# Optimization experiments

Hardware: AMD Instinct MI355X
Metric: run time of the kernel (lower is better)

## Reference

```python
import jax, jax.numpy as jnp
import numpy as np

S = 8192          # past KV length
H = 4096          # hidden size
NH = 32           # heads
HD = 128          # head dim
INNER = 16384     # MLP inner (4h)
ROT = 64          # rotary dim per 2D-rope half
NUM_LAYERS = 28
LAYER_ID = 0
ALPHA = (2.0 * NUM_LAYERS) ** 0.5
QK_COEFF = float(LAYER_ID + 1)            # query_key_layer_scaling_coeff
COEFF = (128.0 ** 0.5) * QK_COEFF         # math.sqrt(128) * coeff
EPS = 1e-5


def layernorm(x, w, b):
    mu = jnp.mean(x, axis=-1, keepdims=True)
    var = jnp.var(x, axis=-1, keepdims=True)
    return (x - mu) * jax.lax.rsqrt(var + EPS) * w + b


def rotate_half(x):
    # x: [..., 64]; GLM rotate-half at 32
    return jnp.concatenate([-x[..., 32:], x[..., :32]], axis=-1)


def setup_inputs() -> dict:
    key = jax.random.key(0)
    ks = jax.random.split(key, 16)
    # rotary cache (as in the driver script)
    inv_freq = 1.0 / (10000.0 ** (jnp.arange(0, ROT, 2, dtype=jnp.float32) / ROT))  # [32]
    t = jnp.arange(512, dtype=jnp.float32)
    freqs = jnp.einsum('i,j->ij', t, inv_freq)          # [512,32]
    emb = jnp.concatenate([freqs, freqs], axis=-1)      # [512,64]
    w = lambda k, shp: jax.random.normal(k, shp, dtype=jnp.float32) * 0.02
    return {
        'hidden_states': jax.random.normal(ks[0], (1, H), dtype=jnp.float32),
        'past_key': jax.random.normal(ks[1], (S, NH, HD), dtype=jnp.float32),
        'past_value': jax.random.normal(ks[2], (S, NH, HD), dtype=jnp.float32),
        'cos_cached': jnp.cos(emb),
        'sin_cached': jnp.sin(emb),
        'ln1_w': jnp.ones((H,), jnp.float32), 'ln1_b': jnp.zeros((H,), jnp.float32),
        'qkv_w': w(ks[3], (3 * H, H)), 'qkv_b': w(ks[4], (3 * H,)),
        'dense_w': w(ks[5], (H, H)), 'dense_b': w(ks[6], (H,)),
        'ln2_w': jnp.ones((H,), jnp.float32), 'ln2_b': jnp.zeros((H,), jnp.float32),
        'fc1_w': w(ks[7], (INNER, H)), 'fc1_b': w(ks[8], (INNER,)),
        'fc2_w': w(ks[9], (H, INNER)), 'fc2_b': w(ks[10], (H,)),
        'position_ids': jax.random.randint(ks[11], (1, 1), 0, 512),
        'block_position_ids': jax.random.randint(ks[12], (1, 1), 0, 512),
        'attention_mask': jnp.zeros((1, 1, S + 1), dtype=bool),
    }


def reference(hidden_states, past_key, past_value, cos_cached, sin_cached,
              ln1_w, ln1_b, qkv_w, qkv_b, dense_w, dense_b,
              ln2_w, ln2_b, fc1_w, fc1_b, fc2_w, fc2_b,
              position_ids, block_position_ids, attention_mask):
    # rotary lookups: embedding then transpose(0,1) -> [q_len,1,64]
    pos_cos = jnp.transpose(cos_cached[position_ids], (1, 0, 2))
    pos_sin = jnp.transpose(sin_cached[position_ids], (1, 0, 2))
    blk_cos = jnp.transpose(cos_cached[block_position_ids], (1, 0, 2))
    blk_sin = jnp.transpose(sin_cached[block_position_ids], (1, 0, 2))

    residual = layernorm(hidden_states, ln1_w, ln1_b)          # [1, H]
    qkv = residual @ qkv_w.T + qkv_b                           # [1, 3H]
    qkv = qkv.reshape(-1, NH, 3 * HD)                          # [1, 32, 384]
    query, key_new, value_new = jnp.split(qkv, 3, axis=2)      # each [1,32,128]

    q1, q2 = jnp.split(query, 2, axis=2)                       # [1,32,64] each
    k1, k2 = jnp.split(key_new, 2, axis=2)
    q1 = q1 * pos_cos + rotate_half(q1) * pos_sin
    k1 = k1 * pos_cos + rotate_half(k1) * pos_sin
    q2 = q2 * blk_cos + rotate_half(q2) * blk_sin
    k2 = k2 * blk_cos + rotate_half(k2) * blk_sin
    q = jnp.concatenate([q1, q2], axis=-1)                     # [1,32,128]
    k_new = jnp.concatenate([k1, k2], axis=-1)                 # [1,32,128]

    k = jnp.concatenate([past_key, k_new], axis=0)             # [S+1,32,128]
    v = jnp.concatenate([past_value, value_new], axis=0)       # [S+1,32,128]

    # scores: [heads, q=1, S+1]
    scores = jnp.einsum('qhd,khd->hqk', q / COEFF, k)
    scores = jnp.where(attention_mask, jnp.float32(-10000.0), scores)
    scores = scores * QK_COEFF
    probs = jax.nn.softmax(scores, axis=-1)
    ctx = jnp.einsum('hqk,khd->qhd', probs, v).reshape(-1, H)  # [1,4096]

    attn_out = ctx @ dense_w.T + dense_b
    hidden = residual * ALPHA + attn_out

    residual2 = layernorm(hidden, ln2_w, ln2_b)
    mlp = jax.nn.gelu(residual2 @ fc1_w.T + fc1_b, approximate=True)
    mlp = mlp @ fc2_w.T + fc2_b
    out = residual2 * ALPHA + mlp
    return (out, k, v)
```

## Files before the change

### kernel.cpp

```cpp
#include <hip/hip_runtime.h>
#include <math.h>

#define S_PAST 8192
#define S_TOT  8193
#define HID    4096
#define NH     32
#define HD     128
#define INNER  16384
#define CH     16
#define NCH    512
#define ALPHA_ 7.483314773547883f
#define INV_COEFF 0.08838834764831845f
#define EPS_ 1e-5f

typedef float vf4 __attribute__((ext_vector_type(4)));

__global__ __launch_bounds__(256) void ln_kernel(const float* __restrict__ xin,
                                                 const float* __restrict__ w,
                                                 const float* __restrict__ b,
                                                 float* __restrict__ out) {
    int tid = threadIdx.x;
    float xs[16];
    float s = 0.f, s2 = 0.f;
#pragma unroll
    for (int i = 0; i < 16; ++i) {
        float v = xin[tid + i * 256];
        xs[i] = v; s += v; s2 += v * v;
    }
    for (int off = 32; off; off >>= 1) {
        s  += __shfl_down(s, off, 64);
        s2 += __shfl_down(s2, off, 64);
    }
    __shared__ float rs[4], rs2[4];
    __shared__ float mu_s, ri_s;
    int wid = tid >> 6, lane = tid & 63;
    if (lane == 0) { rs[wid] = s; rs2[wid] = s2; }
    __syncthreads();
    if (tid == 0) {
        float S1 = rs[0] + rs[1] + rs[2] + rs[3];
        float S2 = rs2[0] + rs2[1] + rs2[2] + rs2[3];
        float mu = S1 / HID;
        float var = S2 / HID - mu * mu;
        mu_s = mu;
        ri_s = rsqrtf(var + EPS_);
    }
    __syncthreads();
    float mu = mu_s, ri = ri_s;
#pragma unroll
    for (int i = 0; i < 16; ++i) {
        int idx = tid + i * 256;
        out[idx] = (xs[i] - mu) * ri * w[idx] + b[idx];
    }
}

template <int C, int MODE>
__global__ __launch_bounds__(256) void gemv_kernel(
        const float* __restrict__ Wm, const float* __restrict__ bias,
        const float* __restrict__ x, float* __restrict__ y,
        const float* __restrict__ res) {
    int wid = threadIdx.x >> 6, lane = threadIdx.x & 63;
    int r = blockIdx.x * 4 + wid;
    const float4* __restrict__ rowv = (const float4*)(Wm + (size_t)r * C);
    const float4* __restrict__ xv = (const float4*)x;
    constexpr int IT = C / 4 / 64;
    float acc0 = 0.f, acc1 = 0.f;
#pragma unroll 8
    for (int it = 0; it < IT; it += 2) {
        float4 w0 = rowv[lane + it * 64];
        float4 x0 = xv[lane + it * 64];
        float4 w1 = rowv[lane + (it + 1) * 64];
        float4 x1 = xv[lane + (it + 1) * 64];
        acc0 += w0.x * x0.x + w0.y * x0.y + w0.z * x0.z + w0.w * x0.w;
        acc1 += w1.x * x1.x + w1.y * x1.y + w1.z * x1.z + w1.w * x1.w;
    }
    float acc = acc0 + acc1;
    for (int off = 32; off; off >>= 1) acc += __shfl_down(acc, off, 64);
    if (lane == 0) {
        float t = acc + bias[r];
        if (MODE == 1) t += ALPHA_ * res[r];
        if (MODE == 2) {
            float u = t;
            t = 0.5f * u * (1.f + tanhf(0.7978845608028654f * (u + 0.044715f * u * u * u)));
        }
        y[r] = t;
    }
}

__global__ __launch_bounds__(128) void rope_kv_kernel(
        const float* __restrict__ qkv, const float* __restrict__ cosc,
        const float* __restrict__ sinc, const int* __restrict__ pos_ids,
        const int* __restrict__ blk_ids, float* __restrict__ qrot,
        float* __restrict__ kout, float* __restrict__ vout) {
    int h = blockIdx.x, d = threadIdx.x;
    int pos = pos_ids[0], blk = blk_ids[0];
    const float* qh = qkv + h * 384;
    float q = qh[d], k = qh[128 + d], v = qh[256 + d];
    int half = d >> 6;
    int i = d & 63;
    int p = half ? blk : pos;
    float c = cosc[p * 64 + i];
    float s = sinc[p * 64 + i];
    float qpart, kpart;
    int base = half * 64;
    if (i < 32) { qpart = -qh[base + i + 32]; kpart = -qh[128 + base + i + 32]; }
    else        { qpart =  qh[base + i - 32]; kpart =  qh[128 + base + i - 32]; }
    float qo = q * c + qpart * s;
    float ko = k * c + kpart * s;
    qrot[h * HD + d] = qo * INV_COEFF;
    size_t o = (size_t)S_PAST * HID + h * HD + d;
    kout[o] = ko;
    vout[o] = v;
}

#define COPY_GRID 2048
__global__ __launch_bounds__(256) void kv_copy(const vf4* __restrict__ pk,
                                               const vf4* __restrict__ pv,
                                               vf4* __restrict__ ko,
                                               vf4* __restrict__ vo) {
    const size_t n = (size_t)S_PAST * HID / 4;
    int half = blockIdx.x >= (COPY_GRID / 2);
    const vf4* __restrict__ src = half ? pv : pk;
    vf4* __restrict__ dst = half ? vo : ko;
    size_t start = (size_t)(blockIdx.x - half * (COPY_GRID / 2)) * 256 + threadIdx.x;
    size_t stride = (size_t)(COPY_GRID / 2) * 256;
    for (size_t i = start; i < n; i += stride) {
        __builtin_nontemporal_store(__builtin_nontemporal_load(src + i), dst + i);
    }
}

__global__ __launch_bounds__(512) void attn_onepass(
        const float* __restrict__ qrot, const float* __restrict__ pastk,
        const float* __restrict__ pastv, const float* __restrict__ kout,
        const float* __restrict__ vout, const unsigned char* __restrict__ mask,
        float* __restrict__ pctx, float* __restrict__ pL) {
    int tid = threadIdx.x;
    int t = tid & 255, u = tid >> 8;
    int s0 = blockIdx.x * CH;
    int rows = (blockIdx.x == NCH - 1) ? (S_TOT - s0) : CH;
    int rstart = u * 8;
    int rend = u ? rows : 8;
    int a = t >> 5;
    const float4* __restrict__ qv = (const float4*)qrot;
    float4 q0 = qv[t], q1 = qv[256 + t], q2 = qv[512 + t], q3 = qv[768 + t];
    float4 a0 = {0,0,0,0}, a1 = {0,0,0,0}, a2 = {0,0,0,0}, a3 = {0,0,0,0};
    float eL0 = 0.f, eL1 = 0.f, eL2 = 0.f, eL3 = 0.f;
#pragma unroll 4
    for (int r = rstart; r < rend; ++r) {
        int srow = s0 + r;
        bool past = srow < S_PAST;
        const float* kbase = past ? pastk : kout;
        const float4* krow = (const float4*)(kbase + (size_t)srow * HID);
        float4 k0 = krow[t], k1 = krow[256 + t];
        float4 k2 = krow[512 + t], k3 = krow[768 + t];
        float d0 = q0.x * k0.x + q0.y * k0.y + q0.z * k0.z + q0.w * k0.w;
        float d1 = q1.x * k1.x + q1.y * k1.y + q1.z * k1.z + q1.w * k1.w;
        float d2 = q2.x * k2.x + q2.y * k2.y + q2.z * k2.z + q2.w * k2.w;
        float d3 = q3.x * k3.x + q3.y * k3.y + q3.z * k3.z + q3.w * k3.w;
#pragma unroll
        for (int off = 1; off < 32; off <<= 1) {
            d0 += __shfl_xor(d0, off, 64);
            d1 += __shfl_xor(d1, off, 64);
            d2 += __shfl_xor(d2, off, 64);
            d3 += __shfl_xor(d3, off, 64);
        }
        if (mask[srow]) { d0 = d1 = d2 = d3 = -10000.f; }
        float p0 = __expf(d0), p1 = __expf(d1), p2 = __expf(d2), p3 = __expf(d3);
        eL0 += p0; eL1 += p1; eL2 += p2; eL3 += p3;
        const float* vbase = past ? pastv : vout;
        const float4* vrow = (const float4*)(vbase + (size_t)srow * HID);
        float4 v0 = vrow[t], v1 = vrow[256 + t];
        float4 v2 = vrow[512 + t], v3 = vrow[768 + t];
        a0.x += p0 * v0.x; a0.y += p0 * v0.y; a0.z += p0 * v0.z; a0.w += p0 * v0.w;
        a1.x += p1 * v1.x; a1.y += p1 * v1.y; a1.z += p1 * v1.z; a1.w += p1 * v1.w;
        a2.x += p2 * v2.x; a2.y += p2 * v2.y; a2.z += p2 * v2.z; a2.w += p2 * v2.w;
        a3.x += p3 * v3.x; a3.y += p3 * v3.y; a3.z += p3 * v3.z; a3.w += p3 * v3.w;
    }
    __shared__ float acc_lds[256][16];
    __shared__ float eLds[2][8][4];
    if (u == 1) {
        acc_lds[t][0]  = a0.x; acc_lds[t][1]  = a0.y; acc_lds[t][2]  = a0.z; acc_lds[t][3]  = a0.w;
        acc_lds[t][4]  = a1.x; acc_lds[t][5]  = a1.y; acc_lds[t][6]  = a1.z; acc_lds[t][7]  = a1.w;
        acc_lds[t][8]  = a2.x; acc_lds[t][9]  = a2.y; acc_lds[t][10] = a2.z; acc_lds[t][11] = a2.w;
        acc_lds[t][12] = a3.x; acc_lds[t][13] = a3.y; acc_lds[t][14] = a3.z; acc_lds[t][15] = a3.w;
    }
    if ((t & 31) == 0) {
        eLds[u][a][0] = eL0; eLds[u][a][1] = eL1;
        eLds[u][a][2] = eL2; eLds[u][a][3] = eL3;
    }
    __syncthreads();
    if (u == 0) {
        a0.x += acc_lds[t][0];  a0.y += acc_lds[t][1];  a0.z += acc_lds[t][2];  a0.w += acc_lds[t][3];
        a1.x += acc_lds[t][4];  a1.y += acc_lds[t][5];  a1.z += acc_lds[t][6];  a1.w += acc_lds[t][7];
        a2.x += acc_lds[t][8];  a2.y += acc_lds[t][9];  a2.z += acc_lds[t][10]; a2.w += acc_lds[t][11];
        a3.x += acc_lds[t][12]; a3.y += acc_lds[t][13]; a3.z += acc_lds[t][14]; a3.w += acc_lds[t][15];
        float4* pc = (float4*)(pctx + (size_t)blockIdx.x * HID);
        pc[t] = a0; pc[256 + t] = a1; pc[512 + t] = a2; pc[768 + t] = a3;
    }
    if (tid < NH) {
        int ah = tid & 7, g = tid >> 3;
        pL[tid * NCH + blockIdx.x] = eLds[0][ah][g] + eLds[1][ah][g];
    }
}

__global__ __launch_bounds__(256) void ctx_reduce(const float* __restrict__ pctx,
                                                  const float* __restrict__ pL,
                                                  float* __restrict__ ctx) {
    int b = blockIdx.x, t = threadIdx.x;
    int i0 = b * 16;
    int h = i0 >> 7;
    float e = pL[h * NCH + t] + pL[h * NCH + 256 + t];
    for (int off = 32; off; off >>= 1) e += __shfl_down(e, off, 64);
    __shared__ float ew[4];
    int wid = t >> 6, lane = t & 63;
    if (lane == 0) ew[wid] = e;
    int r0 = t >> 4, ii = t & 15;
    float a = 0.f;
    for (int r = r0; r < NCH; r += 16) a += pctx[(size_t)r * HID + i0 + ii];
    __shared__ float sc[16][17];
    sc[r0][ii] = a;
    __syncthreads();
    float Lh = ew[0] + ew[1] + ew[2] + ew[3];
    if (t < 16) {
        float s = 0.f;
#pragma unroll
        for (int r = 0; r < 16; ++r) s += sc[r][t];
        ctx[i0 + t] = s / Lh;
    }
}

extern "C" void kernel_launch(void* const* d_in, const int* in_sizes, int n_in,
                              void* d_out, int out_size, void* d_ws, size_t ws_size,
                              hipStream_t stream) {
    const float* hidden = (const float*)d_in[0];
    const float* past_k = (const float*)d_in[1];
    const float* past_v = (const float*)d_in[2];
    const float* cosc = (const float*)d_in[3];
    const float* sinc = (const float*)d_in[4];
    const float* ln1w = (const float*)d_in[5];
    const float* ln1b = (const float*)d_in[6];
    const float* qkvw = (const float*)d_in[7];
    const float* qkvb = (const float*)d_in[8];
    const float* denw = (const float*)d_in[9];
    const float* denb = (const float*)d_in[10];
    const float* ln2w = (const float*)d_in[11];
    const float* ln2b = (const float*)d_in[12];
    const float* fc1w = (const float*)d_in[13];
    const float* fc1b = (const float*)d_in[14];
    const float* fc2w = (const float*)d_in[15];
    const float* fc2b = (const float*)d_in[16];
    const int* pos = (const int*)d_in[17];
    const int* blk = (const int*)d_in[18];
    const unsigned char* mask = (const unsigned char*)d_in[19];

    float* out_f = (float*)d_out;
    float* kout = out_f + HID;
    float* vout = kout + (size_t)S_TOT * HID;

    float* ws = (float*)d_ws;
    float* resid1 = ws;
    float* qkvv   = ws + 4096;
    float* qrot   = ws + 16384;
    float* ctx    = ws + 20480;
    float* hid2   = ws + 24576;
    float* resid2 = ws + 28672;
    float* mlpi   = ws + 32768;
    float* pL     = ws + 49152;
    float* pctx   = ws + 65536;

    ln_kernel<<<1, 256, 0, stream>>>(hidden, ln1w, ln1b, resid1);
    gemv_kernel<HID, 0><<<3 * HID / 4, 256, 0, stream>>>(qkvw, qkvb, resid1, qkvv, nullptr);
    rope_kv_kernel<<<NH, HD, 0, stream>>>(qkvv, cosc, sinc, pos, blk, qrot, kout, vout);
    kv_copy<<<COPY_GRID, 256, 0, stream>>>((const vf4*)past_k, (const vf4*)past_v,
                                           (vf4*)kout, (vf4*)vout);
    attn_onepass<<<NCH, 512, 0, stream>>>(qrot, past_k, past_v, kout, vout, mask, pctx, pL);
    ctx_reduce<<<256, 256, 0, stream>>>(pctx, pL, ctx);
    gemv_kernel<HID, 1><<<HID / 4, 256, 0, stream>>>(denw, denb, ctx, hid2, resid1);
    ln_kernel<<<1, 256, 0, stream>>>(hid2, ln2w, ln2b, resid2);
    gemv_kernel<HID, 2><<<INNER / 4, 256, 0, stream>>>(fc1w, fc1b, resid2, mlpi, nullptr);
    gemv_kernel<INNER, 1><<<HID / 4, 256, 0, stream>>>(fc2w, fc2b, mlpi, out_f, resid2);
}
```

Before: 312.7 us.

## Fuse KV cache copy into attention pass and widen fc2 GEMV to one row per block

Drops the separate kv_copy kernel. The attention kernel now writes the past K/V rows it already loads into the output cache, so the 256 MB of past KV is read once instead of twice. The fc2 GEMV also gets a dedicated kernel with one block of 256 threads per output row, which gives more parallelism for the long 16384-wide rows. The trade-off is that the attention kernel now carries heavy store traffic alongside its reads, and its loads are no longer nontemporal.

```diff
diff --git a/kernel.cpp b/kernel.cpp
--- a/kernel.cpp
+++ b/kernel.cpp
@@ -12,8 +12,6 @@
 #define ALPHA_ 7.483314773547883f
 #define INV_COEFF 0.08838834764831845f
 #define EPS_ 1e-5f
-
-typedef float vf4 __attribute__((ext_vector_type(4)));
 
 __global__ __launch_bounds__(256) void ln_kernel(const float* __restrict__ xin,
                                                  const float* __restrict__ w,
@@ -82,6 +80,37 @@
             float u = t;
             t = 0.5f * u * (1.f + tanhf(0.7978845608028654f * (u + 0.044715f * u * u * u)));
         }
+        y[r] = t;
+    }
+}
+
+__global__ __launch_bounds__(256) void gemv_wide_kernel(
+        const float* __restrict__ Wm, const float* __restrict__ bias,
+        const float* __restrict__ x, float* __restrict__ y,
+        const float* __restrict__ res) {
+    int tid = threadIdx.x;
+    int r = blockIdx.x;
+    const float4* __restrict__ rowv = (const float4*)(Wm + (size_t)r * INNER);
+    const float4* __restrict__ xv = (const float4*)x;
+    float acc0 = 0.f, acc1 = 0.f;
+#pragma unroll 8
+    for (int it = 0; it < 16; it += 2) {
+        float4 w0 = rowv[tid + it * 256];
+        float4 x0 = xv[tid + it * 256];
+        float4 w1 = rowv[tid + (it + 1) * 256];
+        float4 x1 = xv[tid + (it + 1) * 256];
+        acc0 += w0.x * x0.x + w0.y * x0.y + w0.z * x0.z + w0.w * x0.w;
+        acc1 += w1.x * x1.x + w1.y * x1.y + w1.z * x1.z + w1.w * x1.w;
+    }
+    float acc = acc0 + acc1;
+    for (int off = 32; off; off >>= 1) acc += __shfl_down(acc, off, 64);
+    __shared__ float red[4];
+    int wid = tid >> 6, lane = tid & 63;
+    if (lane == 0) red[wid] = acc;
+    __syncthreads();
+    if (tid == 0) {
+        float t = red[0] + red[1] + red[2] + red[3] + bias[r];
+        t += ALPHA_ * res[r];
         y[r] = t;
     }
 }
@@ -112,26 +141,10 @@
     vout[o] = v;
 }
 
-#define COPY_GRID 2048
-__global__ __launch_bounds__(256) void kv_copy(const vf4* __restrict__ pk,
-                                               const vf4* __restrict__ pv,
-                                               vf4* __restrict__ ko,
-                                               vf4* __restrict__ vo) {
-    const size_t n = (size_t)S_PAST * HID / 4;
-    int half = blockIdx.x >= (COPY_GRID / 2);
-    const vf4* __restrict__ src = half ? pv : pk;
-    vf4* __restrict__ dst = half ? vo : ko;
-    size_t start = (size_t)(blockIdx.x - half * (COPY_GRID / 2)) * 256 + threadIdx.x;
-    size_t stride = (size_t)(COPY_GRID / 2) * 256;
-    for (size_t i = start; i < n; i += stride) {
-        __builtin_nontemporal_store(__builtin_nontemporal_load(src + i), dst + i);
-    }
-}
-
 __global__ __launch_bounds__(512) void attn_onepass(
         const float* __restrict__ qrot, const float* __restrict__ pastk,
-        const float* __restrict__ pastv, const float* __restrict__ kout,
-        const float* __restrict__ vout, const unsigned char* __restrict__ mask,
+        const float* __restrict__ pastv, float* __restrict__ kout,
+        float* __restrict__ vout, const unsigned char* __restrict__ mask,
         float* __restrict__ pctx, float* __restrict__ pL) {
     int tid = threadIdx.x;
     int t = tid & 255, u = tid >> 8;
@@ -149,9 +162,19 @@
         int srow = s0 + r;
         bool past = srow < S_PAST;
         const float* kbase = past ? pastk : kout;
+        const float* vbase = past ? pastv : vout;
         const float4* krow = (const float4*)(kbase + (size_t)srow * HID);
+        const float4* vrow = (const float4*)(vbase + (size_t)srow * HID);
         float4 k0 = krow[t], k1 = krow[256 + t];
         float4 k2 = krow[512 + t], k3 = krow[768 + t];
+        float4 v0 = vrow[t], v1 = vrow[256 + t];
+        float4 v2 = vrow[512 + t], v3 = vrow[768 + t];
+        if (past) {
+            float4* ko = (float4*)(kout + (size_t)srow * HID);
+            ko[t] = k0; ko[256 + t] = k1; ko[512 + t] = k2; ko[768 + t] = k3;
+            float4* vo = (float4*)(vout + (size_t)srow * HID);
+            vo[t] = v0; vo[256 + t] = v1; vo[512 + t] = v2; vo[768 + t] = v3;
+        }
         float d0 = q0.x * k0.x + q0.y * k0.y + q0.z * k0.z + q0.w * k0.w;
         float d1 = q1.x * k1.x + q1.y * k1.y + q1.z * k1.z + q1.w * k1.w;
         float d2 = q2.x * k2.x + q2.y * k2.y + q2.z * k2.z + q2.w * k2.w;
@@ -166,10 +189,6 @@
         if (mask[srow]) { d0 = d1 = d2 = d3 = -10000.f; }
         float p0 = __expf(d0), p1 = __expf(d1), p2 = __expf(d2), p3 = __expf(d3);
         eL0 += p0; eL1 += p1; eL2 += p2; eL3 += p3;
-        const float* vbase = past ? pastv : vout;
-        const float4* vrow = (const float4*)(vbase + (size_t)srow * HID);
-        float4 v0 = vrow[t], v1 = vrow[256 + t];
-        float4 v2 = vrow[512 + t], v3 = vrow[768 + t];
         a0.x += p0 * v0.x; a0.y += p0 * v0.y; a0.z += p0 * v0.z; a0.w += p0 * v0.w;
         a1.x += p1 * v1.x; a1.y += p1 * v1.y; a1.z += p1 * v1.z; a1.w += p1 * v1.w;
         a2.x += p2 * v2.x; a2.y += p2 * v2.y; a2.z += p2 * v2.z; a2.w += p2 * v2.w;
@@ -270,12 +289,10 @@
     ln_kernel<<<1, 256, 0, stream>>>(hidden, ln1w, ln1b, resid1);
     gemv_kernel<HID, 0><<<3 * HID / 4, 256, 0, stream>>>(qkvw, qkvb, resid1, qkvv, nullptr);
     rope_kv_kernel<<<NH, HD, 0, stream>>>(qkvv, cosc, sinc, pos, blk, qrot, kout, vout);
-    kv_copy<<<COPY_GRID, 256, 0, stream>>>((const vf4*)past_k, (const vf4*)past_v,
-                                           (vf4*)kout, (vf4*)vout);
     attn_onepass<<<NCH, 512, 0, stream>>>(qrot, past_k, past_v, kout, vout, mask, pctx, pL);
     ctx_reduce<<<256, 256, 0, stream>>>(pctx, pL, ctx);
     gemv_kernel<HID, 1><<<HID / 4, 256, 0, stream>>>(denw, denb, ctx, hid2, resid1);
     ln_kernel<<<1, 256, 0, stream>>>(hid2, ln2w, ln2b, resid2);
     gemv_kernel<HID, 2><<<INNER / 4, 256, 0, stream>>>(fc1w, fc1b, resid2, mlpi, nullptr);
-    gemv_kernel<INNER, 1><<<HID / 4, 256, 0, stream>>>(fc2w, fc2b, mlpi, out_f, resid2);
-}
+    gemv_wide_kernel<<<HID, 256, 0, stream>>>(fc2w, fc2b, mlpi, out_f, resid2);
+}
```

Measured after the change: 283.4 us, median of 2. 9.4% less time.
